# Kernel tuning notes

Hardware: AMD Instinct MI355X
Metric: run time of the kernel (lower is better)

## Reference

```python
import jax, jax.numpy as jnp
import numpy as np

IOU_THRESHOLD = 0.5
BOX_W, OBJ_W, CLS_W = 3.54, 64.3, 37.4
B, N, NS, NA, NC = 16, 32, 3, 3, 80
IMG = 512.0

ANCHORS_PX = np.array([[[10, 13], [16, 30], [33, 23]],
                       [[30, 61], [62, 45], [59, 119]],
                       [[116, 90], [156, 198], [373, 326]]], dtype=np.float32)
STRIDES = np.array([8.0, 16.0, 32.0], dtype=np.float32)


def setup_inputs() -> dict:
    key = jax.random.key(0)
    ks = jax.random.split(key, 6)
    infs = {}
    for s, g in enumerate([64, 32, 16]):
        infs[f"inf{s}"] = jax.random.normal(ks[s], (B, NA, g, g, 5 + NC), dtype=jnp.float32)
    xy = jax.random.uniform(ks[3], (B, N, 2), minval=0.0, maxval=IMG)
    wh = jax.random.uniform(ks[4], (B, N, 2), minval=8.0, maxval=96.0)
    cls_id = jax.random.randint(ks[5], (B, N, 1), 0, NC).astype(jnp.float32)
    targets = jnp.concatenate([xy, wh, cls_id], axis=-1)  # [B,N,5] xywh(px)+class
    return {"inf0": infs["inf0"], "inf1": infs["inf1"], "inf2": infs["inf2"],
            "anchors": jnp.asarray(ANCHORS_PX), "strides": jnp.asarray(STRIDES),
            "targets": targets}


def xywh2rect(b):
    xy, wh = b[..., 0:2], b[..., 2:4]
    return jnp.concatenate([xy - wh / 2, xy + wh / 2], axis=-1)


def jaccard(a1, a2):
    x0 = jnp.maximum(a1[..., 0], a2[..., 0]); y0 = jnp.maximum(a1[..., 1], a2[..., 1])
    x1 = jnp.minimum(a1[..., 2], a2[..., 2]); y1 = jnp.minimum(a1[..., 3], a2[..., 3])
    inter = (x1 - x0) * (y1 - y0) * ((x0 < x1) & (y0 < y1)).astype(a1.dtype)
    area = lambda r: (r[..., 2] - r[..., 0]) * (r[..., 3] - r[..., 1])
    union = area(a1) + area(a2) - inter
    return inter / union


def bce_logits(p, t):
    # pos_weight == 1.0 for both obj and cls heads
    return t * jax.nn.softplus(-p) + (1.0 - t) * jax.nn.softplus(p)


def reference(inf0, inf1, inf2, anchors, strides, targets):
    inference = [inf0, inf1, inf2]
    nb, nt, _ = targets.shape
    ns, na, _ = anchors.shape
    nc = inf0.shape[-1] - 5
    # compress targets: all targets assumed valid (no -1 padding)
    bidx = jnp.repeat(jnp.arange(nb), nt)            # [n]
    flat = targets.reshape(-1, 5)                     # [n,5]
    cls_id = flat[:, 4].astype(jnp.int32)             # [n]
    boxes = flat[:, 0:4]                              # [n,4] xywh px
    # per-scale target boxes in grid units, xy -> cell offset
    tb = boxes[:, None, :] / strides[None, :, None]   # [n,ns,4]
    c = jnp.floor(tb[..., 0:2])
    tb = jnp.concatenate([tb[..., 0:2] - c, tb[..., 2:4]], axis=-1)
    ci = c[..., 0].astype(jnp.int32)                  # [n,ns]
    cj = c[..., 1].astype(jnp.int32)
    # anchors in grid units with center 0.5
    anc = jnp.concatenate([jnp.full((ns, na, 2), 0.5, anchors.dtype),
                           anchors / strides[:, None, None]], axis=-1)
    # anchor matching: [n,ns,na]
    obj = jaccard(xywh2rect(tb)[:, :, None, :], xywh2rect(anc)[None]) > IOU_THRESHOLD
    a_idx = jnp.arange(na)
    box_loss = 0.0; obj_loss = 0.0; cls_loss = 0.0
    for s in range(ns):
        inf = inference[s]                            # [B,na,H,W,5+nc]
        mf = obj[:, s, :].astype(jnp.float32)         # [n,na]
        cnt = jnp.maximum(mf.sum(), 1.0)
        b, cis, cjs = bidx, ci[:, s], cj[:, s]
        pred = inf[b[:, None], a_idx[None, :], cjs[:, None], cis[:, None]]  # [n,na,5+nc]
        # decode box
        p_xy = jax.nn.sigmoid(pred[..., 0:2])
        p_wh = jnp.minimum(jnp.exp(pred[..., 2:4]), 1000.0) * anc[s, :, 2:4][None]
        p_box = jnp.concatenate([p_xy, p_wh], axis=-1)        # [n,na,4]
        t_box = jnp.broadcast_to(tb[:, s, None, :], p_box.shape)
        iou = jaccard(xywh2rect(p_box), xywh2rect(t_box))      # [n,na]
        box_loss = box_loss + jnp.sum((1.0 - iou) * mf) / cnt
        # objectness target: scatter 1 at matched cells
        t_obj = jnp.zeros(inf.shape[:-1], jnp.float32)
        t_obj = t_obj.at[b[:, None], a_idx[None, :], cjs[:, None], cis[:, None]].max(mf)
        obj_loss = obj_loss + jnp.mean(bce_logits(inf[..., 4], t_obj))
        # class loss over matched rows only
        t_cls = jnp.broadcast_to(jax.nn.one_hot(cls_id, nc)[:, None, :], pred[..., 5:].shape)
        cls_bce = bce_logits(pred[..., 5:], t_cls)             # [n,na,nc]
        cls_loss = cls_loss + jnp.sum(cls_bce * mf[..., None]) / (cnt * nc)
    return box_loss * BOX_W + obj_loss * OBJ_W + cls_loss * CLS_W
```

## Files before the change

kernel.cpp:

```cpp
#include <hip/hip_runtime.h>

constexpr int S0 = 16 * 3 * 64 * 64;
constexpr int S1 = 16 * 3 * 32 * 32;
constexpr int S2 = 16 * 3 * 16 * 16;
constexpr int TOT = S0 + S1 + S2;

constexpr int TWAVES  = 512 * 9;
constexpr int TBLOCKS = TWAVES / 4;
constexpr int OBLOCKS = TOT / 256;

constexpr int WS_OBJ = TBLOCKS * 10;

__device__ __forceinline__ float softplusf(float x) {
    return fmaxf(x, 0.0f) + __logf(1.0f + __expf(-fabsf(x)));
}

__device__ __forceinline__ bool anchor_hit(
    float x, float y, float w, float h, float st, float aw, float ah,
    int& ci, int& cj, float& fx, float& fy, float& tbw, float& tbh)
{
    const float tbx = x / st, tby = y / st;
    tbw = w / st; tbh = h / st;
    const float cif = floorf(tbx), cjf = floorf(tby);
    ci = (int)cif; cj = (int)cjf;
    fx = tbx - cif; fy = tby - cjf;
    const float tx0 = fx - tbw*0.5f, ty0 = fy - tbh*0.5f;
    const float tx1 = fx + tbw*0.5f, ty1 = fy + tbh*0.5f;
    const float ax0 = 0.5f - aw*0.5f, ay0 = 0.5f - ah*0.5f;
    const float ax1 = 0.5f + aw*0.5f, ay1 = 0.5f + ah*0.5f;
    const float ix0 = fmaxf(tx0, ax0), iy0 = fmaxf(ty0, ay0);
    const float ix1 = fminf(tx1, ax1), iy1 = fminf(ty1, ay1);
    float inter = (ix1-ix0)*(iy1-iy0);
    inter = (ix0 < ix1 && iy0 < iy1) ? inter : 0.0f;
    const float iou = inter / (tbw*tbh + aw*ah - inter);
    return iou > 0.5f;
}

__global__ __launch_bounds__(256) void yolo_main_kernel(
    const float* __restrict__ inf0, const float* __restrict__ inf1,
    const float* __restrict__ inf2, const float* __restrict__ anchors,
    const float* __restrict__ strides, const float* __restrict__ targets,
    float* __restrict__ ws)
{
    if (blockIdx.x < TBLOCKS) {
        __shared__ float s_part[10];
        if (threadIdx.x < 10) s_part[threadIdx.x] = 0.0f;
        __syncthreads();

        const int wave = blockIdx.x * 4 + (threadIdx.x >> 6);
        const int lane = threadIdx.x & 63;
        const int t  = wave / 9;
        const int sa = wave - 9 * t;
        const int s  = sa / 3;
        const int a  = sa - 3 * s;
        const int b  = t >> 5;

        const float x = targets[t*5+0];
        const float y = targets[t*5+1];
        const float w = targets[t*5+2];
        const float h = targets[t*5+3];
        const int cls = (int)targets[t*5+4];

        const float st = strides[s];
        const float aw = anchors[(s*3+a)*2+0] / st;
        const float ah = anchors[(s*3+a)*2+1] / st;

        int ci, cj; float fx, fy, tbw, tbh;
        const bool hit = anchor_hit(x, y, w, h, st, aw, ah,
                                    ci, cj, fx, fy, tbw, tbh);
        if (hit) {
            const int g = (s == 0) ? 64 : (s == 1) ? 32 : 16;
            const float* inf = (s == 0) ? inf0 : (s == 1) ? inf1 : inf2;
            const float invM = (s == 0) ? 1.0f/(float)S0
                             : (s == 1) ? 1.0f/(float)S1 : 1.0f/(float)S2;

            const int cellflat = ((b*3 + a)*g + cj)*g + ci;
            const float* pred = inf + (long)cellflat * 85;

            const float p4 = pred[4];
            const float px = 1.0f / (1.0f + __expf(-pred[0]));
            const float py = 1.0f / (1.0f + __expf(-pred[1]));
            const float pw = fminf(__expf(pred[2]), 1000.0f) * aw;
            const float ph = fminf(__expf(pred[3]), 1000.0f) * ah;
            const float tx0 = fx - tbw*0.5f, ty0 = fy - tbh*0.5f;
            const float tx1 = fx + tbw*0.5f, ty1 = fy + tbh*0.5f;
            const float bx0 = px - pw*0.5f, by0 = py - ph*0.5f;
            const float bx1 = px + pw*0.5f, by1 = py + ph*0.5f;
            const float jx0 = fmaxf(bx0, tx0), jy0 = fmaxf(by0, ty0);
            const float jx1 = fminf(bx1, tx1), jy1 = fminf(by1, ty1);
            float inter2 = (jx1-jx0)*(jy1-jy0);
            inter2 = (jx0 < jx1 && jy0 < jy1) ? inter2 : 0.0f;
            const float iou2 = inter2 / (pw*ph + tbw*tbh - inter2);

            float v = softplusf(pred[5 + lane]);
            if (lane == cls) v -= pred[5 + cls];
            if (lane < 16) {
                const int c2 = 64 + lane;
                v += softplusf(pred[5 + c2]);
                if (c2 == cls) v -= pred[5 + c2];
            }
            #pragma unroll
            for (int off = 32; off > 0; off >>= 1) v += __shfl_down(v, off, 64);

            bool dup = false;
            if (lane < (t & 31)) {
                const int t2 = (b << 5) + lane;
                const float x2 = targets[t2*5+0];
                const float y2 = targets[t2*5+1];
                const float w2 = targets[t2*5+2];
                const float h2 = targets[t2*5+3];
                int ci2, cj2; float fx2, fy2, tbw2, tbh2;
                const bool hit2 = anchor_hit(x2, y2, w2, h2, st, aw, ah,
                                             ci2, cj2, fx2, fy2, tbw2, tbh2);
                dup = hit2 && (ci2 == ci) && (cj2 == cj);
            }
            const unsigned long long m = __ballot(dup);

            if (lane == 0) {
                atomicAdd(&s_part[1 + s], 1.0f);
                atomicAdd(&s_part[4 + s], 1.0f - iou2);
                atomicAdd(&s_part[7 + s], v);
                if (m == 0ull) atomicAdd(&s_part[0], -p4 * invM);
            }
        }
        __syncthreads();
        if (threadIdx.x < 10)
            ws[blockIdx.x * 10 + threadIdx.x] = s_part[threadIdx.x];
    } else {
        const int bi  = blockIdx.x - TBLOCKS;
        const int idx = bi * 256 + threadIdx.x;
        const float* inf; int local; float w;
        if (idx < S0)           { inf = inf0; local = idx;             w = 1.0f/(float)S0; }
        else if (idx < S0 + S1) { inf = inf1; local = idx - S0;        w = 1.0f/(float)S1; }
        else                    { inf = inf2; local = idx - (S0 + S1); w = 1.0f/(float)S2; }
        float v = softplusf(inf[(long)local * 85 + 4]) * w;
        #pragma unroll
        for (int off = 32; off > 0; off >>= 1) v += __shfl_down(v, off, 64);
        __shared__ float wsum[4];
        const int lane = threadIdx.x & 63, wid = threadIdx.x >> 6;
        if (lane == 0) wsum[wid] = v;
        __syncthreads();
        if (threadIdx.x == 0)
            ws[WS_OBJ + bi] = wsum[0] + wsum[1] + wsum[2] + wsum[3];
    }
}

__global__ __launch_bounds__(256) void yolo_finalize_kernel(
    const float* __restrict__ ws, float* __restrict__ out)
{
    float acc[10];
    #pragma unroll
    for (int c = 0; c < 10; ++c) acc[c] = 0.0f;
    for (int r = threadIdx.x; r < TBLOCKS; r += 256) {
        #pragma unroll
        for (int c = 0; c < 10; ++c) acc[c] += ws[r * 10 + c];
    }
    float obj = 0.0f;
    for (int i = threadIdx.x; i < OBLOCKS; i += 256) obj += ws[WS_OBJ + i];
    acc[0] += obj;

    #pragma unroll
    for (int c = 0; c < 10; ++c) {
        float v = acc[c];
        #pragma unroll
        for (int off = 32; off > 0; off >>= 1) v += __shfl_down(v, off, 64);
        acc[c] = v;
    }
    __shared__ float red[4][10];
    const int lane = threadIdx.x & 63, wid = threadIdx.x >> 6;
    if (lane == 0) {
        #pragma unroll
        for (int c = 0; c < 10; ++c) red[wid][c] = acc[c];
    }
    __syncthreads();
    if (threadIdx.x == 0) {
        float tt[10];
        #pragma unroll
        for (int c = 0; c < 10; ++c)
            tt[c] = red[0][c] + red[1][c] + red[2][c] + red[3][c];
        float box = 0.0f, cls = 0.0f;
        #pragma unroll
        for (int s = 0; s < 3; ++s) {
            const float cnt = fmaxf(tt[1 + s], 1.0f);
            box += tt[4 + s] / cnt;
            cls += tt[7 + s] / (cnt * 80.0f);
        }
        out[0] = 3.54f * box + 64.3f * tt[0] + 37.4f * cls;
    }
}

extern "C" void kernel_launch(void* const* d_in, const int* in_sizes, int n_in,
                              void* d_out, int out_size, void* d_ws, size_t ws_size,
                              hipStream_t stream) {
    const float* inf0    = (const float*)d_in[0];
    const float* inf1    = (const float*)d_in[1];
    const float* inf2    = (const float*)d_in[2];
    const float* anchors = (const float*)d_in[3];
    const float* strides = (const float*)d_in[4];
    const float* targets = (const float*)d_in[5];
    float* ws  = (float*)d_ws;
    float* out = (float*)d_out;

    yolo_main_kernel<<<TBLOCKS + OBLOCKS, 256, 0, stream>>>(
        inf0, inf1, inf2, anchors, strides, targets, ws);
    yolo_finalize_kernel<<<1, 256, 0, stream>>>(ws, out);
}
```

Before: 113.8 us.

## Coarsen objectness reduction to four cells per thread and schedule it first

The dense objectness softplus reduction now has each thread handle four cells, so it uses a quarter as many blocks. It also applies the scale weight once per block instead of once per element. These blocks are now placed before the target-matching blocks in the grid, so the bandwidth-heavy strided loads are issued first. The aim is to cut block-scheduling overhead and keep more loads in flight per thread, with the finalize kernel reading fewer partial sums. The cost is fewer independent blocks to hide latency.

```diff
diff --git a/kernel.cpp b/kernel.cpp
--- a/kernel.cpp
+++ b/kernel.cpp
@@ -5,9 +5,12 @@
 constexpr int S2 = 16 * 3 * 16 * 16;
 constexpr int TOT = S0 + S1 + S2;
 
+constexpr int DBLOCKS = TOT / 1024;
+constexpr int DB0 = S0 / 1024;
+constexpr int DB1 = DB0 + S1 / 1024;
+
 constexpr int TWAVES  = 512 * 9;
 constexpr int TBLOCKS = TWAVES / 4;
-constexpr int OBLOCKS = TOT / 256;
 
 constexpr int WS_OBJ = TBLOCKS * 10;
 
@@ -42,12 +45,33 @@
     const float* __restrict__ strides, const float* __restrict__ targets,
     float* __restrict__ ws)
 {
-    if (blockIdx.x < TBLOCKS) {
+    if (blockIdx.x < DBLOCKS) {
+        const int bi = blockIdx.x;
+        const float* inf; int base; float w;
+        if (bi < DB0)      { inf = inf0; base = bi * 1024;          w = 1.0f/(float)S0; }
+        else if (bi < DB1) { inf = inf1; base = (bi - DB0) * 1024;  w = 1.0f/(float)S1; }
+        else               { inf = inf2; base = (bi - DB1) * 1024;  w = 1.0f/(float)S2; }
+        const int l0 = base + threadIdx.x;
+        const float a0 = inf[(long)(l0      ) * 85 + 4];
+        const float a1 = inf[(long)(l0 + 256) * 85 + 4];
+        const float a2 = inf[(long)(l0 + 512) * 85 + 4];
+        const float a3 = inf[(long)(l0 + 768) * 85 + 4];
+        float v = softplusf(a0) + softplusf(a1) + softplusf(a2) + softplusf(a3);
+        #pragma unroll
+        for (int off = 32; off > 0; off >>= 1) v += __shfl_down(v, off, 64);
+        __shared__ float wsum[4];
+        const int lane = threadIdx.x & 63, wid = threadIdx.x >> 6;
+        if (lane == 0) wsum[wid] = v;
+        __syncthreads();
+        if (threadIdx.x == 0)
+            ws[WS_OBJ + bi] = (wsum[0] + wsum[1] + wsum[2] + wsum[3]) * w;
+    } else {
         __shared__ float s_part[10];
         if (threadIdx.x < 10) s_part[threadIdx.x] = 0.0f;
         __syncthreads();
 
-        const int wave = blockIdx.x * 4 + (threadIdx.x >> 6);
+        const int tb   = blockIdx.x - DBLOCKS;
+        const int wave = tb * 4 + (threadIdx.x >> 6);
         const int lane = threadIdx.x & 63;
         const int t  = wave / 9;
         const int sa = wave - 9 * t;
@@ -125,23 +149,7 @@
         }
         __syncthreads();
         if (threadIdx.x < 10)
-            ws[blockIdx.x * 10 + threadIdx.x] = s_part[threadIdx.x];
-    } else {
-        const int bi  = blockIdx.x - TBLOCKS;
-        const int idx = bi * 256 + threadIdx.x;
-        const float* inf; int local; float w;
-        if (idx < S0)           { inf = inf0; local = idx;             w = 1.0f/(float)S0; }
-        else if (idx < S0 + S1) { inf = inf1; local = idx - S0;        w = 1.0f/(float)S1; }
-        else                    { inf = inf2; local = idx - (S0 + S1); w = 1.0f/(float)S2; }
-        float v = softplusf(inf[(long)local * 85 + 4]) * w;
-        #pragma unroll
-        for (int off = 32; off > 0; off >>= 1) v += __shfl_down(v, off, 64);
-        __shared__ float wsum[4];
-        const int lane = threadIdx.x & 63, wid = threadIdx.x >> 6;
-        if (lane == 0) wsum[wid] = v;
-        __syncthreads();
-        if (threadIdx.x == 0)
-            ws[WS_OBJ + bi] = wsum[0] + wsum[1] + wsum[2] + wsum[3];
+            ws[tb * 10 + threadIdx.x] = s_part[threadIdx.x];
     }
 }
 
@@ -156,7 +164,7 @@
         for (int c = 0; c < 10; ++c) acc[c] += ws[r * 10 + c];
     }
     float obj = 0.0f;
-    for (int i = threadIdx.x; i < OBLOCKS; i += 256) obj += ws[WS_OBJ + i];
+    for (int i = threadIdx.x; i < DBLOCKS; i += 256) obj += ws[WS_OBJ + i];
     acc[0] += obj;
 
     #pragma unroll
@@ -201,7 +209,7 @@
     float* ws  = (float*)d_ws;
     float* out = (float*)d_out;
 
-    yolo_main_kernel<<<TBLOCKS + OBLOCKS, 256, 0, stream>>>(
+    yolo_main_kernel<<<DBLOCKS + TBLOCKS, 256, 0, stream>>>(
         inf0, inf1, inf2, anchors, strides, targets, ws);
     yolo_finalize_kernel<<<1, 256, 0, stream>>>(ws, out);
 }
```

Measured after the change: 113.4 us. About the same (-0.4%).
